# Kernel tuning notes

Measured on AMD Instinct MI355X. Metric: run time of the kernel, lower is better.

Reference implementation:

```python
import jax, jax.numpy as jnp
import numpy as np

B, N, D, L, E = 16, 256, 128, 3, 32768  # graphs, nodes/graph, hidden_dim, num_layers, edges


def _ln(x, g, b, eps=1e-5):
    mu = jnp.mean(x, -1, keepdims=True)
    xc = x - mu
    var = jnp.mean(xc * xc, -1, keepdims=True)
    return xc * jax.lax.rsqrt(var + eps) * g + b


def setup_inputs() -> dict:
    key = jax.random.key(0)
    ks = jax.random.split(key, 16)

    def w(k, shape, fan):
        return jax.random.normal(k, shape, jnp.float32) * (fan ** -0.5)

    x = jax.random.normal(ks[0], (B * N, 1), jnp.float32)
    batch = (jnp.arange(B * N) // N).astype(jnp.int32)
    # E//B edges per graph, endpoints local to that graph (global ids = g*N + local)
    eb = jnp.repeat(jnp.arange(B, dtype=jnp.int32), E // B)
    src = jax.random.randint(ks[1], (E,), 0, N, dtype=jnp.int32)
    dst = jax.random.randint(ks[2], (E,), 0, N, dtype=jnp.int32)
    edge_index = jnp.stack([eb * N + src, eb * N + dst])
    edge_attr = jax.random.normal(ks[3], (E, 1), jnp.float32) * 0.5

    return {
        "x": x,
        "edge_index": edge_index,
        "edge_attr": edge_attr,
        "batch": batch,
        "enc_W": w(ks[4], (1, D), 1),
        "enc_b": jnp.zeros((D,), jnp.float32),
        "msg_W": w(ks[5], (L, 2 * D + 1, D), 2 * D + 1),
        "msg_b": jnp.zeros((L, D), jnp.float32),
        "msg_g": jnp.ones((L, D), jnp.float32),
        "msg_beta": jnp.zeros((L, D), jnp.float32),
        "upd_W": w(ks[6], (L, 2 * D, D), 2 * D),
        "upd_b": jnp.zeros((L, D), jnp.float32),
        "upd_g": jnp.ones((L, D), jnp.float32),
        "upd_beta": jnp.zeros((L, D), jnp.float32),
        "dec_W1": w(ks[7], (2 * D + 1, D), 2 * D + 1),
        "dec_b1": jnp.zeros((D,), jnp.float32),
        "dec_W2": w(ks[8], (D, D // 2), D),
        "dec_b2": jnp.zeros((D // 2,), jnp.float32),
        "dec_W3": w(ks[9], (D // 2, 1), D // 2),
        "dec_b3": jnp.zeros((1,), jnp.float32),
    }


def reference(x, edge_index, edge_attr, batch, enc_W, enc_b,
              msg_W, msg_b, msg_g, msg_beta,
              upd_W, upd_b, upd_g, upd_beta,
              dec_W1, dec_b1, dec_W2, dec_b2, dec_W3, dec_b3):
    n = N
    b = x.shape[0] // n
    # node encoder then dense batch: (B, N, D)
    h = (x @ enc_W + enc_b).reshape(b, n, D)

    src = edge_index[0] % n
    dst = edge_index[1] % n
    eb = batch[edge_index[0]]
    # to_dense_adj (scatter-add duplicates) then symmetrize
    adj = jnp.zeros((b, n, n), h.dtype).at[eb, src, dst].add(edge_attr[:, 0])
    adj = adj + jnp.swapaxes(adj, 1, 2)

    mask = (1.0 - jnp.eye(n, dtype=h.dtype))[None, :, :, None]  # zero self-messages
    for l in range(L):
        # cat([h_target(i), h_source(j), J]) @ W decomposed to avoid the 2D+1 concat
        Wt, Ws, wj = msg_W[l, :D], msg_W[l, D:2 * D], msg_W[l, 2 * D]
        pre = (h @ Wt)[:, :, None, :] + (h @ Ws)[:, None, :, :] \
              + adj[..., None] * wj + msg_b[l]          # (B, N, N, D)
        msgs = jax.nn.silu(_ln(pre, msg_g[l], msg_beta[l]))
        agg = jnp.sum(msgs * mask, axis=2)               # (B, N, D)
        u = jnp.concatenate([h, agg], -1) @ upd_W[l] + upd_b[l]
        h = h + jax.nn.silu(_ln(u, upd_g[l], upd_beta[l]))

    h_src = h[eb, src]
    h_dst = h[eb, dst]
    e = jnp.concatenate([h_src, h_dst, edge_attr], -1)
    e = jax.nn.silu(e @ dec_W1 + dec_b1)
    e = jax.nn.silu(e @ dec_W2 + dec_b2)
    out = jnp.tanh(e @ dec_W3 + dec_b3)
    return out[:, 0]
```

## Files before the change

### kernel.cpp

```cpp
#include <hip/hip_runtime.h>

#define NB 16
#define NN 256
#define DD 128
#define NL 3
#define NE 32768
#define BN 4096

__device__ __forceinline__ float siluf(float y) {
  return __fdividef(y, 1.0f + __expf(-y));
}

template<int CTRL>
__device__ __forceinline__ float dpp_add(float x) {
  int v = __builtin_amdgcn_update_dpp(0, __float_as_int(x), CTRL, 0xF, 0xF, true);
  return x + __int_as_float(v);
}

__device__ __forceinline__ float sum16(float x) {
  x = dpp_add<0xB1>(x);
  x = dpp_add<0x4E>(x);
  x = dpp_add<0x141>(x);
  x = dpp_add<0x140>(x);
  return x;
}

__device__ __forceinline__ float sum32(float x) {
  x = sum16(x);
  int v = __builtin_amdgcn_ds_swizzle(__float_as_int(x), 0x401F);
  return x + __int_as_float(v);
}

__device__ __forceinline__ float sum64(float x) {
  x = sum32(x);
  return x + __shfl_xor(x, 32, 64);
}


__global__ __launch_bounds__(256) void k_zero(float4* __restrict__ p) {
  int t = blockIdx.x * 256 + threadIdx.x;
  float4 z = make_float4(0.f, 0.f, 0.f, 0.f);
  p[t] = z;
  p[t + 131072] = z;
}

__global__ __launch_bounds__(256) void k_encode(
    const float* __restrict__ x, const float* __restrict__ W,
    const float* __restrict__ bb, float* __restrict__ h) {
  int t = blockIdx.x * 256 + threadIdx.x;
  int i = t >> 5;
  int c = (t & 31) << 2;
  float xv = x[i];
  float4 w = *(const float4*)(W + c);
  float4 bv = *(const float4*)(bb + c);
  float4 o;
  o.x = fmaf(xv, w.x, bv.x); o.y = fmaf(xv, w.y, bv.y);
  o.z = fmaf(xv, w.z, bv.z); o.w = fmaf(xv, w.w, bv.w);
  *(float4*)(h + i * DD + c) = o;
}

__global__ __launch_bounds__(256) void k_scatter(
    const int* __restrict__ ei, const float* __restrict__ ea,
    float* __restrict__ adj) {
  int e = blockIdx.x * 256 + threadIdx.x;
  int g0 = ei[e];
  int g1 = ei[NE + e];
  float v = ea[e];
  int b = g0 >> 8;
  int s = g0 & 255;
  int d = g1 & 255;
  atomicAdd(adj + (b * NN + s) * NN + d, v);
  atomicAdd(adj + (b * NN + d) * NN + s, v);
}

__global__ __launch_bounds__(64) void k_wprep(
    const float* __restrict__ msgW, float* __restrict__ wst) {
  int l = blockIdx.x;
  const float* wj = msgW + (size_t)l * (2 * DD + 1) * DD + 2 * DD * DD;
  int d0 = threadIdx.x << 1;
  float2 wv = *(const float2*)(wj + d0);
  float s1 = sum64(wv.x + wv.y);
  float s2 = sum64(fmaf(wv.x, wv.x, wv.y * wv.y));
  if (threadIdx.x == 0)
    *(float2*)(wst + 2 * l) = make_float2(s1 * 0.0078125f, s2 * 0.0078125f);
}

__global__ __launch_bounds__(256) void k_gemm2(
    const float* __restrict__ A, const float* __restrict__ W1,
    const float* __restrict__ W2, const float* __restrict__ bias1,
    const float* __restrict__ wj,
    float* __restrict__ C1, float* __restrict__ C2,
    float* __restrict__ statT, float* __restrict__ statS) {
  __shared__ float sa[8][128];
  int r = threadIdx.x >> 5;
  int c4 = (threadIdx.x & 31) << 2;
  int row0 = blockIdx.x << 3;
  ((float4*)&sa[0][0])[threadIdx.x] = ((const float4*)(A + row0 * DD))[threadIdx.x];
  __syncthreads();
  float4 a1 = {0.f, 0.f, 0.f, 0.f}, a2 = {0.f, 0.f, 0.f, 0.f};
  #pragma unroll 4
  for (int m = 0; m < DD; ++m) {
    float a = sa[r][m];
    float4 w1 = *(const float4*)(W1 + m * DD + c4);
    float4 w2 = *(const float4*)(W2 + m * DD + c4);
    a1.x = fmaf(a, w1.x, a1.x); a1.y = fmaf(a, w1.y, a1.y);
    a1.z = fmaf(a, w1.z, a1.z); a1.w = fmaf(a, w1.w, a1.w);
    a2.x = fmaf(a, w2.x, a2.x); a2.y = fmaf(a, w2.y, a2.y);
    a2.z = fmaf(a, w2.z, a2.z); a2.w = fmaf(a, w2.w, a2.w);
  }
  if (bias1) {
    float4 bv = *(const float4*)(bias1 + c4);
    a1.x += bv.x; a1.y += bv.y; a1.z += bv.z; a1.w += bv.w;
  }
  int rw = row0 + r;
  *(float4*)(C1 + rw * DD + c4) = a1;
  *(float4*)(C2 + rw * DD + c4) = a2;
  if (wj) {
    float4 wv = *(const float4*)(wj + c4);
    float s1t = sum32((a1.x + a1.y) + (a1.z + a1.w));
    float s2t = sum32(fmaf(a1.x, a1.x, a1.y * a1.y) + fmaf(a1.z, a1.z, a1.w * a1.w));
    float s3t = sum32(fmaf(a1.x, wv.x, a1.y * wv.y) + fmaf(a1.z, wv.z, a1.w * wv.w));
    float s1s = sum32((a2.x + a2.y) + (a2.z + a2.w));
    float s2s = sum32(fmaf(a2.x, a2.x, a2.y * a2.y) + fmaf(a2.z, a2.z, a2.w * a2.w));
    float s3s = sum32(fmaf(a2.x, wv.x, a2.y * wv.y) + fmaf(a2.z, wv.z, a2.w * wv.w));
    if ((threadIdx.x & 31) == 0) {
      const float inv = 0.0078125f;
      ((float4*)statT)[rw] = make_float4(s1t * inv, s2t * inv, s3t * inv, 0.f);
      ((float4*)statS)[rw] = make_float4(s1s * inv, s2s * inv, s3s * inv, 0.f);
    }
  }
}

__global__ __launch_bounds__(256) void k_ts(
    const float* __restrict__ T, const float* __restrict__ S,
    const float* __restrict__ adj,
    const float* __restrict__ statT, const float* __restrict__ statS,
    const float* __restrict__ wst, float* __restrict__ MR4) {
  __shared__ float sT[64][64];
  __shared__ float sS[64][64];
  int b = blockIdx.x >> 4;
  int i0 = ((blockIdx.x >> 2) & 3) << 6;
  int j0 = (blockIdx.x & 3) << 6;
  int t = threadIdx.x;
  int ti = t >> 4, tj = t & 15;
  float acc[4][4] = {};
  int sr = t >> 2, scg = t & 3;
  const float* Trow = T + ((size_t)(b * NN + i0 + sr)) * DD + scg * 16;
  const float* Srow = S + ((size_t)(b * NN + j0 + sr)) * DD + scg * 16;
  for (int kc = 0; kc < 2; ++kc) {
    __syncthreads();
    #pragma unroll
    for (int m = 0; m < 4; ++m) {
      float4 v = *(const float4*)(Trow + kc * 64 + m * 4);
      int kk = scg * 16 + m * 4;
      sT[kk + 0][sr] = v.x; sT[kk + 1][sr] = v.y;
      sT[kk + 2][sr] = v.z; sT[kk + 3][sr] = v.w;
      float4 u = *(const float4*)(Srow + kc * 64 + m * 4);
      sS[kk + 0][sr] = u.x; sS[kk + 1][sr] = u.y;
      sS[kk + 2][sr] = u.z; sS[kk + 3][sr] = u.w;
    }
    __syncthreads();
    #pragma unroll 4
    for (int k = 0; k < 64; ++k) {
      float4 rt = *(const float4*)&sT[k][ti << 2];
      float4 rs = *(const float4*)&sS[k][tj << 2];
      acc[0][0] = fmaf(rt.x, rs.x, acc[0][0]);
      acc[0][1] = fmaf(rt.x, rs.y, acc[0][1]);
      acc[0][2] = fmaf(rt.x, rs.z, acc[0][2]);
      acc[0][3] = fmaf(rt.x, rs.w, acc[0][3]);
      acc[1][0] = fmaf(rt.y, rs.x, acc[1][0]);
      acc[1][1] = fmaf(rt.y, rs.y, acc[1][1]);
      acc[1][2] = fmaf(rt.y, rs.z, acc[1][2]);
      acc[1][3] = fmaf(rt.y, rs.w, acc[1][3]);
      acc[2][0] = fmaf(rt.z, rs.x, acc[2][0]);
      acc[2][1] = fmaf(rt.z, rs.y, acc[2][1]);
      acc[2][2] = fmaf(rt.z, rs.z, acc[2][2]);
      acc[2][3] = fmaf(rt.z, rs.w, acc[2][3]);
      acc[3][0] = fmaf(rt.w, rs.x, acc[3][0]);
      acc[3][1] = fmaf(rt.w, rs.y, acc[3][1]);
      acc[3][2] = fmaf(rt.w, rs.z, acc[3][2]);
      acc[3][3] = fmaf(rt.w, rs.w, acc[3][3]);
    }
  }
  float2 ws = *(const float2*)wst;
  float4 stT[4], stS[4];
  #pragma unroll
  for (int o = 0; o < 4; ++o) {
    stT[o] = ((const float4*)statT)[b * NN + i0 + (ti << 2) + o];
    stS[o] = ((const float4*)statS)[b * NN + j0 + (tj << 2) + o];
  }
  #pragma unroll
  for (int oi = 0; oi < 4; ++oi) {
    int row = b * NN + i0 + (ti << 2) + oi;
    float4 av = *(const float4*)(adj + (size_t)row * NN + j0 + (tj << 2));
    float4* m4row = (float4*)MR4 + (size_t)row * NN + j0 + (tj << 2);
    #pragma unroll
    for (int oj = 0; oj < 4; ++oj) {
      float a = (oj == 0) ? av.x : (oj == 1) ? av.y : (oj == 2) ? av.z : av.w;
      float mean = stT[oi].x + stS[oj].x + a * ws.x;
      float e2 = stT[oi].y + stS[oj].y + a * a * ws.y
               + fmaf(acc[oi][oj], 0.015625f, 2.f * a * (stT[oi].z + stS[oj].z));
      float var = fmaf(-mean, mean, e2);
      float Rv = rsqrtf(var + 1e-5f);
      m4row[oj] = make_float4(Rv, -mean * Rv, a, 0.f);
    }
  }
}

__global__ __launch_bounds__(512, 4) void k_messages(
    const float* __restrict__ hT, const float* __restrict__ hS,
    const float* __restrict__ MR4, const float* __restrict__ wj,
    const float* __restrict__ mg, const float* __restrict__ mbe,
    float* __restrict__ agg) {
  __shared__ float4 smr[4 * 256];
  const float LN2 = 0.6931471805599453f;
  const float L2E = 1.4426950408889634f;
  int b = blockIdx.x >> 6;
  int i0 = (blockIdx.x & 63) << 2;
  int t = threadIdx.x;
  int w = t >> 6, lane = t & 63;
  int p = w >> 2;
  int q = w & 3;
  int half = lane >> 5, li = lane & 31;
  int iloc = (p << 1) + half;
  int i = i0 + iloc;
  int row = b * NN + i;
  int d0 = li << 2;
  float4 tv = *(const float4*)(hT + (size_t)row * DD + d0);
  float4 wv = *(const float4*)(wj + d0);
  float4 gv = *(const float4*)(mg + d0);
  float4 be = *(const float4*)(mbe + d0);
  float G0 = gv.x * L2E, G1 = gv.y * L2E, G2 = gv.z * L2E, G3 = gv.w * L2E;
  float B0 = be.x * L2E, B1 = be.y * L2E, B2 = be.z * L2E, B3 = be.w * L2E;
  float a0 = 0.f, a1 = 0.f, a2 = 0.f, a3 = 0.f;

  {
    const float4* msrc = (const float4*)MR4 + (size_t)(b * NN + i0) * NN;
    smr[t] = msrc[t];
    smr[t + 512] = msrc[t + 512];
  }
  __syncthreads();

  const float4* mrow = smr + (iloc << 8) + (q << 6);
  const float4* hrow = (const float4*)(hS + (size_t)(b * NN + (q << 6)) * DD) + li;

  #pragma unroll 4
  for (int jj = 0; jj < 64; ++jj) {
    float4 m4 = mrow[jj];
    float4 hs = hrow[jj << 5];
    float v0 = fmaf(m4.z, wv.x, tv.x + hs.x);
    float v1 = fmaf(m4.z, wv.y, tv.y + hs.y);
    float v2 = fmaf(m4.z, wv.z, tv.z + hs.z);
    float v3 = fmaf(m4.z, wv.w, tv.w + hs.w);
    float z0 = fmaf(m4.x, v0, m4.y);
    float z1 = fmaf(m4.x, v1, m4.y);
    float z2 = fmaf(m4.x, v2, m4.y);
    float z3 = fmaf(m4.x, v3, m4.y);
    float y0 = fmaf(G0, z0, B0);
    float y1 = fmaf(G1, z1, B1);
    float y2 = fmaf(G2, z2, B2);
    float y3 = fmaf(G3, z3, B3);
    float e0 = __builtin_amdgcn_exp2f(-y0);
    float e1 = __builtin_amdgcn_exp2f(-y1);
    float e2 = __builtin_amdgcn_exp2f(-y2);
    float e3 = __builtin_amdgcn_exp2f(-y3);
    float d0v = 1.0f + e0, d1v = 1.0f + e1;
    float d2v = 1.0f + e2, d3v = 1.0f + e3;
    float r01 = __builtin_amdgcn_rcpf(d0v * d1v);
    float r23 = __builtin_amdgcn_rcpf(d2v * d3v);
    a0 = fmaf(y0 * d1v, r01, a0);
    a1 = fmaf(y1 * d0v, r01, a1);
    a2 = fmaf(y2 * d3v, r23, a2);
    a3 = fmaf(y3 * d2v, r23, a3);
  }
  if ((i >> 6) == q) {
    float4 m4 = smr[(iloc << 8) + i];
    float4 hs = ((const float4*)(hS + (size_t)(b * NN + i) * DD))[li];
    float v0 = fmaf(m4.z, wv.x, tv.x + hs.x);
    float v1 = fmaf(m4.z, wv.y, tv.y + hs.y);
    float v2 = fmaf(m4.z, wv.z, tv.z + hs.z);
    float v3 = fmaf(m4.z, wv.w, tv.w + hs.w);
    float z0 = fmaf(m4.x, v0, m4.y);
    float z1 = fmaf(m4.x, v1, m4.y);
    float z2 = fmaf(m4.x, v2, m4.y);
    float z3 = fmaf(m4.x, v3, m4.y);
    float y0 = fmaf(G0, z0, B0);
    float y1 = fmaf(G1, z1, B1);
    float y2 = fmaf(G2, z2, B2);
    float y3 = fmaf(G3, z3, B3);
    float e0 = __builtin_amdgcn_exp2f(-y0);
    float e1 = __builtin_amdgcn_exp2f(-y1);
    float e2 = __builtin_amdgcn_exp2f(-y2);
    float e3 = __builtin_amdgcn_exp2f(-y3);
    float d0v = 1.0f + e0, d1v = 1.0f + e1;
    float d2v = 1.0f + e2, d3v = 1.0f + e3;
    float r01 = __builtin_amdgcn_rcpf(d0v * d1v);
    float r23 = __builtin_amdgcn_rcpf(d2v * d3v);
    a0 = fmaf(y0 * d1v, -r01, a0);
    a1 = fmaf(y1 * d0v, -r01, a1);
    a2 = fmaf(y2 * d3v, -r23, a2);
    a3 = fmaf(y3 * d2v, -r23, a3);
  }
  __syncthreads();
  float4* smg = (float4*)smr;
  smg[(((iloc << 2) + q) << 5) + li] = make_float4(a0, a1, a2, a3);
  __syncthreads();
  if (t < 128) {
    int il2 = t >> 5, l2 = t & 31;
    float4 s0 = smg[(((il2 << 2) + 0) << 5) + l2];
    float4 s1 = smg[(((il2 << 2) + 1) << 5) + l2];
    float4 s2 = smg[(((il2 << 2) + 2) << 5) + l2];
    float4 s3 = smg[(((il2 << 2) + 3) << 5) + l2];
    float4 o;
    o.x = ((s0.x + s1.x) + (s2.x + s3.x)) * LN2;
    o.y = ((s0.y + s1.y) + (s2.y + s3.y)) * LN2;
    o.z = ((s0.z + s1.z) + (s2.z + s3.z)) * LN2;
    o.w = ((s0.w + s1.w) + (s2.w + s3.w)) * LN2;
    *(float4*)(agg + (size_t)(b * NN + i0 + il2) * DD + (l2 << 2)) = o;
  }
}

__global__ __launch_bounds__(256) void k_update(
    float* __restrict__ h, const float* __restrict__ agg,
    const float* __restrict__ W, const float* __restrict__ ub,
    const float* __restrict__ ug, const float* __restrict__ ube) {
  __shared__ float scat[8][256];
  int r = threadIdx.x >> 5;
  int c4 = (threadIdx.x & 31) << 2;
  int row0 = blockIdx.x << 3;
  {
    int t = threadIdx.x;
    float4 v = ((const float4*)(h + row0 * DD))[t];
    int f = t << 2; int rr = f >> 7; int mm = f & 127;
    *(float4*)&scat[rr][mm] = v;
    float4 va = ((const float4*)(agg + row0 * DD))[t];
    *(float4*)&scat[rr][DD + mm] = va;
  }
  __syncthreads();
  float4 acc = *(const float4*)(ub + c4);
  #pragma unroll 4
  for (int m = 0; m < 2 * DD; ++m) {
    float a = scat[r][m];
    float4 wv = *(const float4*)(W + m * DD + c4);
    acc.x = fmaf(a, wv.x, acc.x);
    acc.y = fmaf(a, wv.y, acc.y);
    acc.z = fmaf(a, wv.z, acc.z);
    acc.w = fmaf(a, wv.w, acc.w);
  }
  float s1 = sum32((acc.x + acc.y) + (acc.z + acc.w));
  float s2 = sum32(fmaf(acc.x, acc.x, acc.y * acc.y) + fmaf(acc.z, acc.z, acc.w * acc.w));
  float mean = s1 * 0.0078125f;
  float var = fmaf(-mean, mean, s2 * 0.0078125f);
  float rstd = rsqrtf(var + 1e-5f);
  float4 g  = *(const float4*)(ug + c4);
  float4 be = *(const float4*)(ube + c4);
  float4 ho = *(const float4*)&scat[r][c4];
  float4 o;
  o.x = ho.x + siluf(fmaf((acc.x - mean) * rstd, g.x, be.x));
  o.y = ho.y + siluf(fmaf((acc.y - mean) * rstd, g.y, be.y));
  o.z = ho.z + siluf(fmaf((acc.z - mean) * rstd, g.z, be.z));
  o.w = ho.w + siluf(fmaf((acc.w - mean) * rstd, g.w, be.w));
  *(float4*)(h + (row0 + r) * DD + c4) = o;
}

__global__ __launch_bounds__(256, 2) void k_decoder(
    const int* __restrict__ ei, const float* __restrict__ ea,
    const float* __restrict__ P, const float* __restrict__ Q,
    const float* __restrict__ w1e, const float* __restrict__ b1,
    const float* __restrict__ W2, const float* __restrict__ b2,
    const float* __restrict__ W3, const float* __restrict__ b3,
    float* __restrict__ out) {
  __shared__ float sS[64][132];
  int t = threadIdx.x;
  {
    int e = t >> 2, qq = t & 3;
    int eg = (blockIdx.x << 6) + e;
    int g0 = ei[eg], g1 = ei[NE + eg];
    float av = ea[eg];
    const float4* p4 = (const float4*)(P + (size_t)g0 * DD + qq * 32);
    const float4* q4 = (const float4*)(Q + (size_t)g1 * DD + qq * 32);
    const float4* w4 = (const float4*)(w1e + qq * 32);
    const float4* b4 = (const float4*)(b1 + qq * 32);
    #pragma unroll
    for (int m = 0; m < 8; ++m) {
      float4 p = p4[m], qv = q4[m], wv = w4[m], bv = b4[m];
      float4 sv;
      sv.x = siluf(fmaf(av, wv.x, (p.x + qv.x) + bv.x));
      sv.y = siluf(fmaf(av, wv.y, (p.y + qv.y) + bv.y));
      sv.z = siluf(fmaf(av, wv.z, (p.z + qv.z) + bv.z));
      sv.w = siluf(fmaf(av, wv.w, (p.w + qv.w) + bv.w));
      *(float4*)&sS[e][(qq << 5) + (m << 2)] = sv;
    }
  }
  __syncthreads();
  int ti = t >> 4, tj = t & 15;
  float4 acc[4] = {{0.f,0.f,0.f,0.f},{0.f,0.f,0.f,0.f},{0.f,0.f,0.f,0.f},{0.f,0.f,0.f,0.f}};
  const float4* W2g = (const float4*)W2;
  #pragma unroll 4
  for (int k4 = 0; k4 < 32; ++k4) {
    float4 sv[4], wv[4];
    #pragma unroll
    for (int r = 0; r < 4; ++r)
      sv[r] = *(const float4*)&sS[(ti << 2) + r][k4 << 2];
    #pragma unroll
    for (int kk = 0; kk < 4; ++kk)
      wv[kk] = W2g[(((k4 << 2) + kk) << 4) + tj];
    #pragma unroll
    for (int r = 0; r < 4; ++r) {
      acc[r].x = fmaf(sv[r].x, wv[0].x, acc[r].x);
      acc[r].y = fmaf(sv[r].x, wv[0].y, acc[r].y);
      acc[r].z = fmaf(sv[r].x, wv[0].z, acc[r].z);
      acc[r].w = fmaf(sv[r].x, wv[0].w, acc[r].w);
      acc[r].x = fmaf(sv[r].y, wv[1].x, acc[r].x);
      acc[r].y = fmaf(sv[r].y, wv[1].y, acc[r].y);
      acc[r].z = fmaf(sv[r].y, wv[1].z, acc[r].z);
      acc[r].w = fmaf(sv[r].y, wv[1].w, acc[r].w);
      acc[r].x = fmaf(sv[r].z, wv[2].x, acc[r].x);
      acc[r].y = fmaf(sv[r].z, wv[2].y, acc[r].y);
      acc[r].z = fmaf(sv[r].z, wv[2].z, acc[r].z);
      acc[r].w = fmaf(sv[r].z, wv[2].w, acc[r].w);
      acc[r].x = fmaf(sv[r].w, wv[3].x, acc[r].x);
      acc[r].y = fmaf(sv[r].w, wv[3].y, acc[r].y);
      acc[r].z = fmaf(sv[r].w, wv[3].z, acc[r].z);
      acc[r].w = fmaf(sv[r].w, wv[3].w, acc[r].w);
    }
  }
  float4 b2v = *(const float4*)(b2 + (tj << 2));
  float4 w3v = *(const float4*)(W3 + (tj << 2));
  float b3v = b3[0];
  #pragma unroll
  for (int r = 0; r < 4; ++r) {
    float part = siluf(acc[r].x + b2v.x) * w3v.x;
    part = fmaf(siluf(acc[r].y + b2v.y), w3v.y, part);
    part = fmaf(siluf(acc[r].z + b2v.z), w3v.z, part);
    part = fmaf(siluf(acc[r].w + b2v.w), w3v.w, part);
    part = sum16(part);
    if (tj == 0)
      out[(blockIdx.x << 6) + (ti << 2) + r] = tanhf(part + b3v);
  }
}

extern "C" void kernel_launch(void* const* d_in, const int* in_sizes, int n_in,
                              void* d_out, int out_size, void* d_ws, size_t ws_size,
                              hipStream_t stream) {
  const float* x     = (const float*)d_in[0];
  const int*   ei    = (const int*)  d_in[1];
  const float* ea    = (const float*)d_in[2];
  const float* encW  = (const float*)d_in[4];
  const float* encb  = (const float*)d_in[5];
  const float* msgW  = (const float*)d_in[6];
  const float* msgb  = (const float*)d_in[7];
  const float* msgg  = (const float*)d_in[8];
  const float* msgbe = (const float*)d_in[9];
  const float* updW  = (const float*)d_in[10];
  const float* updb  = (const float*)d_in[11];
  const float* updg  = (const float*)d_in[12];
  const float* updbe = (const float*)d_in[13];
  const float* dW1   = (const float*)d_in[14];
  const float* db1   = (const float*)d_in[15];
  const float* dW2   = (const float*)d_in[16];
  const float* db2   = (const float*)d_in[17];
  const float* dW3   = (const float*)d_in[18];
  const float* db3   = (const float*)d_in[19];
  float* out = (float*)d_out;

  float* h     = (float*)d_ws;
  float* adj   = h     + BN * DD;
  float* hT    = adj   + NB * NN * NN;
  float* hS    = hT    + BN * DD;
  float* agg   = hS    + BN * DD;
  float* statT = agg   + BN * DD;
  float* statS = statT + BN * 4;
  float* wst   = statS + BN * 4;
  float* MR4   = wst   + 8;

  k_zero<<<512, 256, 0, stream>>>((float4*)adj);
  k_encode<<<512, 256, 0, stream>>>(x, encW, encb, h);
  k_scatter<<<NE / 256, 256, 0, stream>>>(ei, ea, adj);
  k_wprep<<<NL, 64, 0, stream>>>(msgW, wst);

  for (int l = 0; l < NL; ++l) {
    const float* Wl = msgW + (size_t)l * (2 * DD + 1) * DD;
    const float* wjl = Wl + 2 * DD * DD;
    k_gemm2<<<BN / 8, 256, 0, stream>>>(h, Wl, Wl + DD * DD, msgb + l * DD, wjl,
                                        hT, hS, statT, statS);
    k_ts<<<256, 256, 0, stream>>>(hT, hS, adj, statT, statS, wst + 2 * l, MR4);
    k_messages<<<1024, 512, 0, stream>>>(hT, hS, MR4, wjl,
        msgg + l * DD, msgbe + l * DD, agg);
    k_update<<<BN / 8, 256, 0, stream>>>(h, agg, updW + (size_t)l * 2 * DD * DD,
        updb + l * DD, updg + l * DD, updbe + l * DD);
  }

  k_gemm2<<<BN / 8, 256, 0, stream>>>(h, dW1, dW1 + DD * DD, nullptr, nullptr,
                                      hT, hS, statT, statS);
  k_decoder<<<NE / 64, 256, 0, stream>>>(ei, ea, hT, hS, dW1 + 2 * DD * DD, db1,
      dW2, db2, dW3, db3, out);
}
```

Baseline: 315.3 us.

## Fuse node update into message kernel and merge setup kernels

The per-layer update GEMM, LayerNorm and residual are folded into the message-aggregation kernel. Each block keeps its 4 rows of h and the aggregated messages in shared memory, splits the 256-long reduction across 4 thread segments, and combines the partial sums before writing h directly. This removes the agg round trip through global memory and one launch per layer. Zeroing, encoding and weight-stat prep are also merged into one kernel. In exchange each block uses more shared memory and adds extra barriers, which may lower occupancy of the message kernel.

Result: slower. 412.3 us (+30.8%).

```diff
diff --git a/kernel.cpp b/kernel.cpp
--- a/kernel.cpp
+++ b/kernel.cpp
@@ -37,26 +37,34 @@
 }
 
 
-__global__ __launch_bounds__(256) void k_zero(float4* __restrict__ p) {
+__global__ __launch_bounds__(256) void k_pre(
+    const float* __restrict__ x, const float* __restrict__ encW,
+    const float* __restrict__ encb, const float* __restrict__ msgW,
+    float* __restrict__ h, float* __restrict__ adj, float* __restrict__ wst) {
   int t = blockIdx.x * 256 + threadIdx.x;
   float4 z = make_float4(0.f, 0.f, 0.f, 0.f);
-  p[t] = z;
-  p[t + 131072] = z;
-}
-
-__global__ __launch_bounds__(256) void k_encode(
-    const float* __restrict__ x, const float* __restrict__ W,
-    const float* __restrict__ bb, float* __restrict__ h) {
-  int t = blockIdx.x * 256 + threadIdx.x;
+  float4* a4 = (float4*)adj;
+  a4[t] = z;
+  a4[t + 131072] = z;
   int i = t >> 5;
   int c = (t & 31) << 2;
   float xv = x[i];
-  float4 w = *(const float4*)(W + c);
-  float4 bv = *(const float4*)(bb + c);
+  float4 w = *(const float4*)(encW + c);
+  float4 bv = *(const float4*)(encb + c);
   float4 o;
   o.x = fmaf(xv, w.x, bv.x); o.y = fmaf(xv, w.y, bv.y);
   o.z = fmaf(xv, w.z, bv.z); o.w = fmaf(xv, w.w, bv.w);
-  *(float4*)(h + i * DD + c) = o;
+  *(float4*)(h + (size_t)i * DD + c) = o;
+  if (blockIdx.x < NL && threadIdx.x < 64) {
+    int l = blockIdx.x;
+    const float* wj = msgW + (size_t)l * (2 * DD + 1) * DD + 2 * DD * DD;
+    int d0 = threadIdx.x << 1;
+    float2 wv = *(const float2*)(wj + d0);
+    float s1 = sum64(wv.x + wv.y);
+    float s2 = sum64(fmaf(wv.x, wv.x, wv.y * wv.y));
+    if (threadIdx.x == 0)
+      *(float2*)(wst + 2 * l) = make_float2(s1 * 0.0078125f, s2 * 0.0078125f);
+  }
 }
 
 __global__ __launch_bounds__(256) void k_scatter(
@@ -73,18 +81,6 @@
   atomicAdd(adj + (b * NN + d) * NN + s, v);
 }
 
-__global__ __launch_bounds__(64) void k_wprep(
-    const float* __restrict__ msgW, float* __restrict__ wst) {
-  int l = blockIdx.x;
-  const float* wj = msgW + (size_t)l * (2 * DD + 1) * DD + 2 * DD * DD;
-  int d0 = threadIdx.x << 1;
-  float2 wv = *(const float2*)(wj + d0);
-  float s1 = sum64(wv.x + wv.y);
-  float s2 = sum64(fmaf(wv.x, wv.x, wv.y * wv.y));
-  if (threadIdx.x == 0)
-    *(float2*)(wst + 2 * l) = make_float2(s1 * 0.0078125f, s2 * 0.0078125f);
-}
-
 __global__ __launch_bounds__(256) void k_gemm2(
     const float* __restrict__ A, const float* __restrict__ W1,
     const float* __restrict__ W2, const float* __restrict__ bias1,
@@ -95,7 +91,7 @@
   int r = threadIdx.x >> 5;
   int c4 = (threadIdx.x & 31) << 2;
   int row0 = blockIdx.x << 3;
-  ((float4*)&sa[0][0])[threadIdx.x] = ((const float4*)(A + row0 * DD))[threadIdx.x];
+  ((float4*)&sa[0][0])[threadIdx.x] = ((const float4*)(A + (size_t)row0 * DD))[threadIdx.x];
   __syncthreads();
   float4 a1 = {0.f, 0.f, 0.f, 0.f}, a2 = {0.f, 0.f, 0.f, 0.f};
   #pragma unroll 4
@@ -113,8 +109,8 @@
     a1.x += bv.x; a1.y += bv.y; a1.z += bv.z; a1.w += bv.w;
   }
   int rw = row0 + r;
-  *(float4*)(C1 + rw * DD + c4) = a1;
-  *(float4*)(C2 + rw * DD + c4) = a2;
+  *(float4*)(C1 + (size_t)rw * DD + c4) = a1;
+  *(float4*)(C2 + (size_t)rw * DD + c4) = a2;
   if (wj) {
     float4 wv = *(const float4*)(wj + c4);
     float s1t = sum32((a1.x + a1.y) + (a1.z + a1.w));
@@ -207,12 +203,16 @@
   }
 }
 
-__global__ __launch_bounds__(512, 4) void k_messages(
+__global__ __launch_bounds__(512, 4) void k_msgupd(
     const float* __restrict__ hT, const float* __restrict__ hS,
     const float* __restrict__ MR4, const float* __restrict__ wj,
     const float* __restrict__ mg, const float* __restrict__ mbe,
-    float* __restrict__ agg) {
+    float* __restrict__ h, const float* __restrict__ uW,
+    const float* __restrict__ ub, const float* __restrict__ ug,
+    const float* __restrict__ ube) {
   __shared__ float4 smr[4 * 256];
+  __shared__ float scat[4][256];
+  __shared__ float4 pbuf[4][4][32];
   const float LN2 = 0.6931471805599453f;
   const float L2E = 1.4426950408889634f;
   int b = blockIdx.x >> 6;
@@ -238,6 +238,11 @@
     const float4* msrc = (const float4*)MR4 + (size_t)(b * NN + i0) * NN;
     smr[t] = msrc[t];
     smr[t + 512] = msrc[t + 512];
+    if (t < 128) {
+      int r2 = t >> 5, l2 = t & 31;
+      *(float4*)&scat[r2][l2 << 2] =
+          *(const float4*)(h + (size_t)(b * NN + i0 + r2) * DD + (l2 << 2));
+    }
   }
   __syncthreads();
 
@@ -316,51 +321,57 @@
     o.y = ((s0.y + s1.y) + (s2.y + s3.y)) * LN2;
     o.z = ((s0.z + s1.z) + (s2.z + s3.z)) * LN2;
     o.w = ((s0.w + s1.w) + (s2.w + s3.w)) * LN2;
-    *(float4*)(agg + (size_t)(b * NN + i0 + il2) * DD + (l2 << 2)) = o;
-  }
-}
-
-__global__ __launch_bounds__(256) void k_update(
-    float* __restrict__ h, const float* __restrict__ agg,
-    const float* __restrict__ W, const float* __restrict__ ub,
-    const float* __restrict__ ug, const float* __restrict__ ube) {
-  __shared__ float scat[8][256];
-  int r = threadIdx.x >> 5;
-  int c4 = (threadIdx.x & 31) << 2;
-  int row0 = blockIdx.x << 3;
+    *(float4*)&scat[il2][DD + (l2 << 2)] = o;
+  }
+  __syncthreads();
   {
-    int t = threadIdx.x;
-    float4 v = ((const float4*)(h + row0 * DD))[t];
-    int f = t << 2; int rr = f >> 7; int mm = f & 127;
-    *(float4*)&scat[rr][mm] = v;
-    float4 va = ((const float4*)(agg + row0 * DD))[t];
-    *(float4*)&scat[rr][DD + mm] = va;
-  }
-  __syncthreads();
-  float4 acc = *(const float4*)(ub + c4);
-  #pragma unroll 4
-  for (int m = 0; m < 2 * DD; ++m) {
-    float a = scat[r][m];
-    float4 wv = *(const float4*)(W + m * DD + c4);
-    acc.x = fmaf(a, wv.x, acc.x);
-    acc.y = fmaf(a, wv.y, acc.y);
-    acc.z = fmaf(a, wv.z, acc.z);
-    acc.w = fmaf(a, wv.w, acc.w);
-  }
-  float s1 = sum32((acc.x + acc.y) + (acc.z + acc.w));
-  float s2 = sum32(fmaf(acc.x, acc.x, acc.y * acc.y) + fmaf(acc.z, acc.z, acc.w * acc.w));
-  float mean = s1 * 0.0078125f;
-  float var = fmaf(-mean, mean, s2 * 0.0078125f);
-  float rstd = rsqrtf(var + 1e-5f);
-  float4 g  = *(const float4*)(ug + c4);
-  float4 be = *(const float4*)(ube + c4);
-  float4 ho = *(const float4*)&scat[r][c4];
-  float4 o;
-  o.x = ho.x + siluf(fmaf((acc.x - mean) * rstd, g.x, be.x));
-  o.y = ho.y + siluf(fmaf((acc.y - mean) * rstd, g.y, be.y));
-  o.z = ho.z + siluf(fmaf((acc.z - mean) * rstd, g.z, be.z));
-  o.w = ho.w + siluf(fmaf((acc.w - mean) * rstd, g.w, be.w));
-  *(float4*)(h + (row0 + r) * DD + c4) = o;
+    int r2 = t >> 7;
+    int cq = (t >> 2) & 31;
+    int seg = t & 3;
+    int c4u = cq << 2;
+    const float* Wb = uW + (size_t)(seg << 6) * DD;
+    float4 pacc = {0.f, 0.f, 0.f, 0.f};
+    #pragma unroll 4
+    for (int m4 = 0; m4 < 16; ++m4) {
+      float4 av = *(const float4*)&scat[r2][(seg << 6) + (m4 << 2)];
+      #pragma unroll
+      for (int k = 0; k < 4; ++k) {
+        float a_ = (k == 0) ? av.x : (k == 1) ? av.y : (k == 2) ? av.z : av.w;
+        float4 wvv = *(const float4*)(Wb + ((m4 << 2) + k) * DD + c4u);
+        pacc.x = fmaf(a_, wvv.x, pacc.x);
+        pacc.y = fmaf(a_, wvv.y, pacc.y);
+        pacc.z = fmaf(a_, wvv.z, pacc.z);
+        pacc.w = fmaf(a_, wvv.w, pacc.w);
+      }
+    }
+    pbuf[r2][seg][cq] = pacc;
+  }
+  __syncthreads();
+  if (t < 128) {
+    int rr = t >> 5, l2 = t & 31;
+    float4 p0 = pbuf[rr][0][l2], p1 = pbuf[rr][1][l2];
+    float4 p2 = pbuf[rr][2][l2], p3 = pbuf[rr][3][l2];
+    float4 ubv = *(const float4*)(ub + (l2 << 2));
+    float4 u;
+    u.x = ubv.x + (p0.x + p1.x) + (p2.x + p3.x);
+    u.y = ubv.y + (p0.y + p1.y) + (p2.y + p3.y);
+    u.z = ubv.z + (p0.z + p1.z) + (p2.z + p3.z);
+    u.w = ubv.w + (p0.w + p1.w) + (p2.w + p3.w);
+    float s1 = sum32((u.x + u.y) + (u.z + u.w));
+    float s2 = sum32(fmaf(u.x, u.x, u.y * u.y) + fmaf(u.z, u.z, u.w * u.w));
+    float mean = s1 * 0.0078125f;
+    float var = fmaf(-mean, mean, s2 * 0.0078125f);
+    float rstd = rsqrtf(var + 1e-5f);
+    float4 g  = *(const float4*)(ug + (l2 << 2));
+    float4 b2 = *(const float4*)(ube + (l2 << 2));
+    float4 ho = *(const float4*)&scat[rr][l2 << 2];
+    float4 o;
+    o.x = ho.x + siluf(fmaf((u.x - mean) * rstd, g.x, b2.x));
+    o.y = ho.y + siluf(fmaf((u.y - mean) * rstd, g.y, b2.y));
+    o.z = ho.z + siluf(fmaf((u.z - mean) * rstd, g.z, b2.z));
+    o.w = ho.w + siluf(fmaf((u.w - mean) * rstd, g.w, b2.w));
+    *(float4*)(h + (size_t)(b * NN + i0 + rr) * DD + (l2 << 2)) = o;
+  }
 }
 
 __global__ __launch_bounds__(256, 2) void k_decoder(
@@ -383,12 +394,12 @@
     const float4* b4 = (const float4*)(b1 + qq * 32);
     #pragma unroll
     for (int m = 0; m < 8; ++m) {
-      float4 p = p4[m], qv = q4[m], wv = w4[m], bv = b4[m];
+      float4 p = p4[m], qv = q4[m], wvv = w4[m], bv = b4[m];
       float4 sv;
-      sv.x = siluf(fmaf(av, wv.x, (p.x + qv.x) + bv.x));
-      sv.y = siluf(fmaf(av, wv.y, (p.y + qv.y) + bv.y));
-      sv.z = siluf(fmaf(av, wv.z, (p.z + qv.z) + bv.z));
-      sv.w = siluf(fmaf(av, wv.w, (p.w + qv.w) + bv.w));
+      sv.x = siluf(fmaf(av, wvv.x, (p.x + qv.x) + bv.x));
+      sv.y = siluf(fmaf(av, wvv.y, (p.y + qv.y) + bv.y));
+      sv.z = siluf(fmaf(av, wvv.z, (p.z + qv.z) + bv.z));
+      sv.w = siluf(fmaf(av, wvv.w, (p.w + qv.w) + bv.w));
       *(float4*)&sS[e][(qq << 5) + (m << 2)] = sv;
     }
   }
@@ -398,31 +409,31 @@
   const float4* W2g = (const float4*)W2;
   #pragma unroll 4
   for (int k4 = 0; k4 < 32; ++k4) {
-    float4 sv[4], wv[4];
+    float4 sv[4], wvv[4];
     #pragma unroll
     for (int r = 0; r < 4; ++r)
       sv[r] = *(const float4*)&sS[(ti << 2) + r][k4 << 2];
     #pragma unroll
     for (int kk = 0; kk < 4; ++kk)
-      wv[kk] = W2g[(((k4 << 2) + kk) << 4) + tj];
+      wvv[kk] = W2g[(((k4 << 2) + kk) << 4) + tj];
     #pragma unroll
     for (int r = 0; r < 4; ++r) {
-      acc[r].x = fmaf(sv[r].x, wv[0].x, acc[r].x);
-      acc[r].y = fmaf(sv[r].x, wv[0].y, acc[r].y);
-      acc[r].z = fmaf(sv[r].x, wv[0].z, acc[r].z);
-      acc[r].w = fmaf(sv[r].x, wv[0].w, acc[r].w);
-      acc[r].x = fmaf(sv[r].y, wv[1].x, acc[r].x);
-      acc[r].y = fmaf(sv[r].y, wv[1].y, acc[r].y);
-      acc[r].z = fmaf(sv[r].y, wv[1].z, acc[r].z);
-      acc[r].w = fmaf(sv[r].y, wv[1].w, acc[r].w);
-      acc[r].x = fmaf(sv[r].z, wv[2].x, acc[r].x);
-      acc[r].y = fmaf(sv[r].z, wv[2].y, acc[r].y);
-      acc[r].z = fmaf(sv[r].z, wv[2].z, acc[r].z);
-      acc[r].w = fmaf(sv[r].z, wv[2].w, acc[r].w);
-      acc[r].x = fmaf(sv[r].w, wv[3].x, acc[r].x);
-      acc[r].y = fmaf(sv[r].w, wv[3].y, acc[r].y);
-      acc[r].z = fmaf(sv[r].w, wv[3].z, acc[r].z);
-      acc[r].w = fmaf(sv[r].w, wv[3].w, acc[r].w);
+      acc[r].x = fmaf(sv[r].x, wvv[0].x, acc[r].x);
+      acc[r].y = fmaf(sv[r].x, wvv[0].y, acc[r].y);
+      acc[r].z = fmaf(sv[r].x, wvv[0].z, acc[r].z);
+      acc[r].w = fmaf(sv[r].x, wvv[0].w, acc[r].w);
+      acc[r].x = fmaf(sv[r].y, wvv[1].x, acc[r].x);
+      acc[r].y = fmaf(sv[r].y, wvv[1].y, acc[r].y);
+      acc[r].z = fmaf(sv[r].y, wvv[1].z, acc[r].z);
+      acc[r].w = fmaf(sv[r].y, wvv[1].w, acc[r].w);
+      acc[r].x = fmaf(sv[r].z, wvv[2].x, acc[r].x);
+      acc[r].y = fmaf(sv[r].z, wvv[2].y, acc[r].y);
+      acc[r].z = fmaf(sv[r].z, wvv[2].z, acc[r].z);
+      acc[r].w = fmaf(sv[r].z, wvv[2].w, acc[r].w);
+      acc[r].x = fmaf(sv[r].w, wvv[3].x, acc[r].x);
+      acc[r].y = fmaf(sv[r].w, wvv[3].y, acc[r].y);
+      acc[r].z = fmaf(sv[r].w, wvv[3].z, acc[r].z);
+      acc[r].w = fmaf(sv[r].w, wvv[3].w, acc[r].w);
     }
   }
   float4 b2v = *(const float4*)(b2 + (tj << 2));
@@ -468,16 +479,13 @@
   float* adj   = h     + BN * DD;
   float* hT    = adj   + NB * NN * NN;
   float* hS    = hT    + BN * DD;
-  float* agg   = hS    + BN * DD;
-  float* statT = agg   + BN * DD;
+  float* statT = hS    + BN * DD;
   float* statS = statT + BN * 4;
   float* wst   = statS + BN * 4;
   float* MR4   = wst   + 8;
 
-  k_zero<<<512, 256, 0, stream>>>((float4*)adj);
-  k_encode<<<512, 256, 0, stream>>>(x, encW, encb, h);
+  k_pre<<<512, 256, 0, stream>>>(x, encW, encb, msgW, h, adj, wst);
   k_scatter<<<NE / 256, 256, 0, stream>>>(ei, ea, adj);
-  k_wprep<<<NL, 64, 0, stream>>>(msgW, wst);
 
   for (int l = 0; l < NL; ++l) {
     const float* Wl = msgW + (size_t)l * (2 * DD + 1) * DD;
@@ -485,9 +493,8 @@
     k_gemm2<<<BN / 8, 256, 0, stream>>>(h, Wl, Wl + DD * DD, msgb + l * DD, wjl,
                                         hT, hS, statT, statS);
     k_ts<<<256, 256, 0, stream>>>(hT, hS, adj, statT, statS, wst + 2 * l, MR4);
-    k_messages<<<1024, 512, 0, stream>>>(hT, hS, MR4, wjl,
-        msgg + l * DD, msgbe + l * DD, agg);
-    k_update<<<BN / 8, 256, 0, stream>>>(h, agg, updW + (size_t)l * 2 * DD * DD,
+    k_msgupd<<<1024, 512, 0, stream>>>(hT, hS, MR4, wjl,
+        msgg + l * DD, msgbe + l * DD, h, updW + (size_t)l * 2 * DD * DD,
         updb + l * DD, updg + l * DD, updbe + l * DD);
   }
 
```
